# Kernel tuning notes

Hardware: AMD Instinct MI355X
Metric: run time of the kernel (lower is better)

The kernel has to match this reference:

```python
import jax, jax.numpy as jnp
import numpy as np

D_MODEL = 2048
H = 16
D_K = D_MODEL // H


def setup_inputs() -> dict:
    key = jax.random.key(0)
    ks = jax.random.split(key, 9)
    b, n, d = 2, 2048, D_MODEL
    s = 1.0 / np.sqrt(d)
    return {
        "x": jax.random.normal(ks[0], (b, n, d), jnp.float32),
        "Wq": jax.random.normal(ks[1], (d, d), jnp.float32) * s,
        "bq": jax.random.normal(ks[2], (d,), jnp.float32) * 0.01,
        "Wk": jax.random.normal(ks[3], (d, d), jnp.float32) * s,
        "bk": jax.random.normal(ks[4], (d,), jnp.float32) * 0.01,
        "Wv": jax.random.normal(ks[5], (d, d), jnp.float32) * s,
        "bv": jax.random.normal(ks[6], (d,), jnp.float32) * 0.01,
        "Wo": jax.random.normal(ks[7], (d, d), jnp.float32) * s,
        "bo": jax.random.normal(ks[8], (d,), jnp.float32) * 0.01,
    }


def reference(x, Wq, bq, Wk, bk, Wv, bv, Wo, bo):
    b, n, d = x.shape
    h, dk = H, D_K

    def split_heads(t):
        return t.reshape(b, n, h, dk).transpose(0, 2, 1, 3)  # (b,h,n,dk)

    q = split_heads(x @ Wq + bq)
    k = split_heads(x @ Wk + bk)
    v = split_heads(x @ Wv + bv)

    scores = jnp.einsum("bhqd,bhkd->bhqk", q, k) / jnp.sqrt(jnp.float32(dk))
    causal = jnp.tril(jnp.ones((n, n), dtype=bool))  # (n,n)
    scores = jnp.where(causal[None, None], scores, -jnp.inf)
    attn = jax.nn.softmax(scores, axis=-1)  # dropout = identity (eval)

    out = jnp.einsum("bhqk,bhkd->bhqd", attn, v)
    out = out.transpose(0, 2, 1, 3).reshape(b, n, d)
    return out @ Wo + bo
```

## Files before the change

kernel.cpp:

```cpp
#include <hip/hip_runtime.h>

typedef unsigned short u16;
typedef unsigned int u32;
typedef __attribute__((ext_vector_type(8))) short short8;
typedef __attribute__((ext_vector_type(4))) float f32x4;
typedef __attribute__((ext_vector_type(16))) float f32x16;
typedef __attribute__((ext_vector_type(4))) u16 u16x4;
typedef __attribute__((ext_vector_type(4))) u32 u32x4;

#define QK_SCALE 0.12751736915185197f

__device__ __forceinline__ u16 f2bf(float f) {
  u32 u = __builtin_bit_cast(u32, f);
  u = u + 0x7FFFu + ((u >> 16) & 1u);
  return (u16)(u >> 16);
}

__device__ __forceinline__ void async_copy16(const void* g, void* l) {
  __builtin_amdgcn_global_load_lds(
      (const __attribute__((address_space(1))) u32*)g,
      (__attribute__((address_space(3))) u32*)l, 16, 0, 0);
}

#define VMCNT(n) asm volatile("s_waitcnt vmcnt(" #n ")" ::: "memory")

__global__ __launch_bounds__(256) void cast_x_kernel(const float* __restrict__ x,
                                                     u16* __restrict__ xb, int n) {
  int i = (blockIdx.x * 256 + threadIdx.x) * 8;
  if (i >= n) return;
  float4 a = *(const float4*)(x + i);
  float4 b = *(const float4*)(x + i + 4);
  short8 o;
  o[0] = (short)f2bf(a.x); o[1] = (short)f2bf(a.y);
  o[2] = (short)f2bf(a.z); o[3] = (short)f2bf(a.w);
  o[4] = (short)f2bf(b.x); o[5] = (short)f2bf(b.y);
  o[6] = (short)f2bf(b.z); o[7] = (short)f2bf(b.w);
  *(short8*)(xb + i) = o;
}

__global__ __launch_bounds__(256) void transW_kernel(
    const float* __restrict__ W0, const float* __restrict__ W1,
    const float* __restrict__ W2, const float* __restrict__ W3,
    u16* __restrict__ O0, u16* __restrict__ O1, u16* __restrict__ O2, u16* __restrict__ O3) {
  const float* Ws[4] = {W0, W1, W2, W3};
  u16* Os[4] = {O0, O1, O2, O3};
  const float* W = Ws[blockIdx.z];
  u16* O = Os[blockIdx.z];

  __shared__ float T[64][65];
  int t = threadIdx.x;
  int k0 = blockIdx.y * 64, n0 = blockIdx.x * 64;
  int r = t >> 4, c = (t & 15) * 4;
#pragma unroll
  for (int i = 0; i < 4; ++i) {
    float4 v = *(const float4*)&W[(size_t)(k0 + r + i * 16) * 2048 + n0 + c];
    T[r + i * 16][c + 0] = v.x; T[r + i * 16][c + 1] = v.y;
    T[r + i * 16][c + 2] = v.z; T[r + i * 16][c + 3] = v.w;
  }
  __syncthreads();
#pragma unroll
  for (int i = 0; i < 4; ++i) {
    int nn = r + i * 16;
    u16x4 o;
    o[0] = f2bf(T[c + 0][nn]); o[1] = f2bf(T[c + 1][nn]);
    o[2] = f2bf(T[c + 2][nn]); o[3] = f2bf(T[c + 3][nn]);
    *(u16x4*)&O[(size_t)(n0 + nn) * 2048 + k0 + c] = o;
  }
}

__global__ __launch_bounds__(256) void transV_kernel(const u16* __restrict__ V,
                                                     u16* __restrict__ Vt) {
  int bh = blockIdx.y;
  int n0 = blockIdx.x * 64;
  const u16* Vb = V + (size_t)bh * 262144;
  u16* Ob = Vt + (size_t)bh * 262144;
  __shared__ u16 T[64 * 129];
  int t = threadIdx.x;
#pragma unroll
  for (int j = 0; j < 4; ++j) {
    int p = t + j * 256;
    int r = p >> 4, c = (p & 15) * 8;
    short8 v = *(const short8*)(Vb + (size_t)(n0 + r) * 128 + c);
#pragma unroll
    for (int e = 0; e < 8; ++e) T[r * 129 + c + e] = (u16)v[e];
  }
  __syncthreads();
#pragma unroll
  for (int pass = 0; pass < 4; ++pass) {
    int dk = (t >> 3) + pass * 32;
    int cn = (t & 7) * 8;
    short8 o;
#pragma unroll
    for (int e = 0; e < 8; ++e) o[e] = (short)T[(cn + e) * 129 + dk];
    *(short8*)(Ob + (size_t)dk * 2048 + n0 + cn) = o;
  }
}

__global__ __launch_bounds__(512, 2) void gemm256_kernel(
    const u16* __restrict__ A, const u16* __restrict__ W,
    const float* __restrict__ b0, const float* __restrict__ b1, const float* __restrict__ b2,
    u16* __restrict__ oq, u16* __restrict__ ok, u16* __restrict__ ov) {
  __shared__ __align__(16) u16 SM[65536];

  int t = threadIdx.x;
  int lane = t & 63, w = t >> 6;
  int wm = w >> 2, wn = w & 3;
  int g = lane >> 4, lr = lane & 15;
  int m0 = blockIdx.y * 256, n0 = blockIdx.x * 256;

  const u16* AsrcB = A + (size_t)(m0 + (t >> 3)) * 2048 + ((t & 7) ^ ((t >> 3) & 7)) * 8;
  const u16* BsrcB = W + (size_t)(n0 + (t >> 3)) * 2048 + ((t & 7) ^ ((t >> 3) & 7)) * 8;
  int t8 = t * 8;

  int ko0 = (g ^ (lr & 7)) * 8;
  int ko1 = ((4 + g) ^ (lr & 7)) * 8;
  int aoff[8], boff[4];
#pragma unroll
  for (int mf = 0; mf < 8; ++mf) aoff[mf] = (wm * 128 + mf * 16 + lr) * 64;
#pragma unroll
  for (int nf = 0; nf < 4; ++nf) boff[nf] = (wn * 64 + nf * 16 + lr) * 64;

  f32x4 acc[8][4] = {};
  short8 af[2][2], bfr[4][2];

#define SA(b, j, tl) \
  async_copy16(AsrcB + (size_t)(j) * 131072 + (tl) * 64, (void*)(SM + (b) * 32768 + (j) * 4096 + t8))
#define SB(b, j, tl) \
  async_copy16(BsrcB + (size_t)(j) * 131072 + (tl) * 64, \
               (void*)(SM + (b) * 32768 + 16384 + (j) * 4096 + t8))

#define PHASE(hbuf, q, STAGE_OPS, VM_OP)                                        \
  {                                                                             \
    const u16* Ab = SM + (hbuf) * 32768;                                        \
    const u16* Bb = Ab + 16384;                                                 \
    af[0][0] = *(const short8*)&Ab[aoff[2 * (q)] + ko0];                        \
    af[0][1] = *(const short8*)&Ab[aoff[2 * (q)] + ko1];                        \
    af[1][0] = *(const short8*)&Ab[aoff[2 * (q) + 1] + ko0];                    \
    af[1][1] = *(const short8*)&Ab[aoff[2 * (q) + 1] + ko1];                    \
    if ((q) == 0) {                                                             \
      _Pragma("unroll") for (int nf = 0; nf < 4; ++nf) {                        \
        bfr[nf][0] = *(const short8*)&Bb[boff[nf] + ko0];                       \
        bfr[nf][1] = *(const short8*)&Bb[boff[nf] + ko1];                       \
      }                                                                         \
    }                                                                           \
    STAGE_OPS;                                                                  \
    __builtin_amdgcn_s_barrier();                                               \
    asm volatile("s_waitcnt lgkmcnt(0)" ::: "memory");                          \
    __builtin_amdgcn_sched_barrier(0);                                          \
    __builtin_amdgcn_s_setprio(1);                                              \
    _Pragma("unroll") for (int kk = 0; kk < 2; ++kk)                            \
        _Pragma("unroll") for (int m2 = 0; m2 < 2; ++m2)                        \
            _Pragma("unroll") for (int nf = 0; nf < 4; ++nf)                    \
                acc[2 * (q) + m2][nf] = __builtin_amdgcn_mfma_f32_16x16x32_bf16(\
                    af[m2][kk], bfr[nf][kk], acc[2 * (q) + m2][nf], 0, 0, 0);   \
    __builtin_amdgcn_s_setprio(0);                                              \
    VM_OP;                                                                      \
    __builtin_amdgcn_s_barrier();                                               \
  }

  SB(0, 0, 0); SB(0, 1, 0); SB(0, 2, 0); SB(0, 3, 0);
  SA(0, 0, 0); SA(0, 2, 0); SA(0, 1, 0); SA(0, 3, 0);
  SB(1, 0, 1); SB(1, 1, 1); SB(1, 2, 1); SB(1, 3, 1);
  SA(1, 0, 1); SA(1, 2, 1);
  VMCNT(6);
  __builtin_amdgcn_s_barrier();

  for (int i = 0; i < 16; ++i) {
    bool more = i < 15;
    int t1 = 2 * i + 1, t2 = 2 * i + 2, t3 = 2 * i + 3;
    PHASE(0, 0, { SA(1, 1, t1); SA(1, 3, t1); }, {});
    PHASE(0, 1, { if (more) { SB(0, 0, t2); SB(0, 1, t2); } }, {});
    PHASE(0, 2, { if (more) { SB(0, 2, t2); SB(0, 3, t2); } }, {});
    PHASE(0, 3, { if (more) { SA(0, 0, t2); SA(0, 2, t2); } },
          { if (more) { VMCNT(6); } else { VMCNT(0); } });
    PHASE(1, 0, { if (more) { SA(0, 1, t2); SA(0, 3, t2); } }, {});
    PHASE(1, 1, { if (more) { SB(1, 0, t3); SB(1, 1, t3); } }, {});
    PHASE(1, 2, { if (more) { SB(1, 2, t3); SB(1, 3, t3); } }, {});
    PHASE(1, 3, { if (more) { SA(1, 0, t3); SA(1, 2, t3); } },
          { if (more) { VMCNT(6); } else { VMCNT(0); } });
  }
#undef PHASE
#undef SA
#undef SB

  int zsel = n0 >> 11;
  const float* bias = (zsel == 0) ? b0 : (zsel == 1) ? b1 : b2;
  u16* outb = (zsel == 0) ? oq : (zsel == 1) ? ok : ov;
#pragma unroll
  for (int mf = 0; mf < 8; ++mf) {
#pragma unroll
    for (int nf = 0; nf < 4; ++nf) {
      int col = n0 + wn * 64 + nf * 16 + lr;
      int cc = col & 2047;
      float bv = bias[cc];
#pragma unroll
      for (int i = 0; i < 4; ++i) {
        int rr = m0 + wm * 128 + mf * 16 + 4 * g + i;
        float v = acc[mf][nf][i] + bv;
        int b = rr >> 11, np = rr & 2047, h = cc >> 7, dk = cc & 127;
        outb[((size_t)(b * 16 + h) * 2048 + np) * 128 + dk] = f2bf(v);
      }
    }
  }
}

__global__ __launch_bounds__(512, 2) void gemmO_kernel(
    const u16* __restrict__ A, const u16* __restrict__ W,
    const float* __restrict__ bias, float* __restrict__ of) {
  __shared__ __align__(16) u16 SM[73728];

  int t = threadIdx.x;
  int lane = t & 63, w = t >> 6;
  int wm = w >> 2, wn = w & 3;
  int g = lane >> 4, lr = lane & 15;
  int m0 = blockIdx.y * 128, n0 = blockIdx.x * 256;

  int sArow = ((t >> 8) << 6) + ((t >> 3) & 31);
  int c8A = (t & 7) ^ ((t >> 3) & 7);
  const u16* Asrc = A + (size_t)(m0 + sArow) * 2048 + c8A * 8;
  int rB = t >> 3;
  int c8B = (t & 7) ^ (rB & 7);
  const u16* Bsrc = W + (size_t)(n0 + rB) * 2048 + c8B * 8;

  int ko0 = (g ^ (lr & 7)) * 8;
  int ko1 = ((4 + g) ^ (lr & 7)) * 8;
  int offA[4], offB[4];
#pragma unroll
  for (int mf = 0; mf < 4; ++mf)
    offA[mf] = (mf >> 1) * 4096 + wm * 2048 + ((mf & 1) * 16 + lr) * 64;
#pragma unroll
  for (int nf = 0; nf < 4; ++nf)
    offB[nf] = 8192 + (wn >> 1) * 8192 + ((wn & 1) * 64 + nf * 16 + lr) * 64;

  f32x4 acc[4][4] = {};

#define STG_A(sbuf, mh, kt) \
  async_copy16(Asrc + (mh) * 65536 + (kt), (void*)(SM + (sbuf) + (mh) * 4096 + t * 8))
#define STG_B(sbuf, half, kt)                                                 \
  do {                                                                        \
    async_copy16(Bsrc + (half) * 262144 + (kt),                               \
                 (void*)(SM + (sbuf) + 8192 + (half) * 8192 + t * 8));        \
    async_copy16(Bsrc + (half) * 262144 + 131072 + (kt),                      \
                 (void*)(SM + (sbuf) + 8192 + (half) * 8192 + 4096 + t * 8)); \
  } while (0)

  STG_A(0, 0, 0); STG_B(0, 0, 0);
  STG_A(0, 1, 0); STG_B(0, 1, 0);
  STG_A(24576, 0, 64); STG_B(24576, 0, 64);
  STG_A(24576, 1, 64); STG_B(24576, 1, 64);
  VMCNT(6);
  __builtin_amdgcn_s_barrier();

  u32 cb = 0, sb = 49152;
  for (int tt = 0; tt < 32; ++tt) {
    int kt2 = (tt + 2) << 6;
    bool stg = tt < 30;
    const u16* Bu = SM + cb;

    short8 af[2][2], bfr[4][2];
#pragma unroll
    for (int m2 = 0; m2 < 2; ++m2) {
      af[m2][0] = *(const short8*)&Bu[offA[m2] + ko0];
      af[m2][1] = *(const short8*)&Bu[offA[m2] + ko1];
    }
#pragma unroll
    for (int nf = 0; nf < 4; ++nf) {
      bfr[nf][0] = *(const short8*)&Bu[offB[nf] + ko0];
      bfr[nf][1] = *(const short8*)&Bu[offB[nf] + ko1];
    }
    if (stg) { STG_A(sb, 0, kt2); STG_B(sb, 0, kt2); }
    __builtin_amdgcn_s_barrier();
    asm volatile("s_waitcnt lgkmcnt(0)" ::: "memory");
    __builtin_amdgcn_sched_barrier(0);
    __builtin_amdgcn_s_setprio(1);
#pragma unroll
    for (int kk = 0; kk < 2; ++kk)
#pragma unroll
      for (int m2 = 0; m2 < 2; ++m2)
#pragma unroll
        for (int nf = 0; nf < 4; ++nf)
          acc[m2][nf] =
              __builtin_amdgcn_mfma_f32_16x16x32_bf16(af[m2][kk], bfr[nf][kk], acc[m2][nf], 0, 0, 0);
    __builtin_amdgcn_s_setprio(0);
    __builtin_amdgcn_s_barrier();

#pragma unroll
    for (int m2 = 0; m2 < 2; ++m2) {
      af[m2][0] = *(const short8*)&Bu[offA[2 + m2] + ko0];
      af[m2][1] = *(const short8*)&Bu[offA[2 + m2] + ko1];
    }
    if (stg) { STG_A(sb, 1, kt2); STG_B(sb, 1, kt2); }
    __builtin_amdgcn_s_barrier();
    asm volatile("s_waitcnt lgkmcnt(0)" ::: "memory");
    __builtin_amdgcn_sched_barrier(0);
    __builtin_amdgcn_s_setprio(1);
#pragma unroll
    for (int kk = 0; kk < 2; ++kk)
#pragma unroll
      for (int m2 = 0; m2 < 2; ++m2)
#pragma unroll
        for (int nf = 0; nf < 4; ++nf)
          acc[2 + m2][nf] = __builtin_amdgcn_mfma_f32_16x16x32_bf16(af[m2][kk], bfr[nf][kk],
                                                                    acc[2 + m2][nf], 0, 0, 0);
    __builtin_amdgcn_s_setprio(0);
    if (tt < 30) { VMCNT(6); } else { VMCNT(0); }
    __builtin_amdgcn_s_barrier();

    cb += 24576; if (cb == 73728) cb = 0;
    sb += 24576; if (sb == 73728) sb = 0;
  }
#undef STG_A
#undef STG_B

#pragma unroll
  for (int mf = 0; mf < 4; ++mf) {
#pragma unroll
    for (int nf = 0; nf < 4; ++nf) {
      int col = n0 + wn * 64 + nf * 16 + lr;
      float bv = bias[col];
#pragma unroll
      for (int i = 0; i < 4; ++i) {
        int rr = m0 + wm * 64 + mf * 16 + 4 * g + i;
        of[(size_t)rr * 2048 + col] = acc[mf][nf][i] + bv;
      }
    }
  }
}

__global__ __launch_bounds__(256, 2) void attn_kernel(
    const u16* __restrict__ Q, const u16* __restrict__ K, const u16* __restrict__ Vt,
    u16* __restrict__ ctx) {
  int bh = blockIdx.y;
  int q0 = (int)(gridDim.x - 1 - blockIdx.x) * 128;
  int t = threadIdx.x, lane = t & 63, w = t >> 6;
  int h = lane >> 5;
  int ql = lane & 31;
  int q0w = q0 + w * 32;
  int qg = q0w + ql;

  const u16* Qb = Q + (size_t)bh * 262144;
  const u16* Kb = K + (size_t)bh * 262144;
  const u16* Vb = Vt + (size_t)bh * 262144;

  __shared__ __align__(16) u16 SM[32768];

  short8 qf[8];
  {
    const u16* qrow = Qb + (size_t)qg * 128 + 8 * h;
#pragma unroll
    for (int kk = 0; kk < 8; ++kk) qf[kk] = *(const short8*)(qrow + 16 * kk);
  }

  f32x16 acc[4] = {};
  float m = -1e30f, lsum = 0.f;

  int nt = (q0 + 128) >> 6;
  int wave_max = q0w + 31;

  auto STAGE = [&](int buf, int kv0) {
    u16* Ksb = SM + buf * 16384;
    u16* Vsb = Ksb + 8192;
#pragma unroll
    for (int it = 0; it < 4; ++it) {
      int p = t + 256 * it;
      int row = p >> 4;
      int c = (p & 15) ^ (row & 15);
      async_copy16(Kb + (size_t)(kv0 + row) * 128 + c * 8, (void*)(Ksb + p * 8));
      async_copy16(Vb + (size_t)(2 * row + (c >> 3)) * 2048 + kv0 + (c & 7) * 8,
                   (void*)(Vsb + p * 8));
    }
  };

  STAGE(0, 0);
  __syncthreads();

  for (int step = 0; step < nt; ++step) {
    int kv0 = step << 6;
    int cur = step & 1;
    if (step + 1 < nt) STAGE(cur ^ 1, (step + 1) << 6);

    if (kv0 <= wave_max) {
      const u16* Ksb = SM + cur * 16384;
      const u16* Vsb = Ksb + 8192;

      f32x16 s0 = {}, s1 = {};
#pragma unroll
      for (int kk = 0; kk < 8; ++kk) {
        int c = (2 * kk + h) ^ (ql & 15);
        short8 kf0 = *(const short8*)&Ksb[ql * 128 + c * 8];
        s0 = __builtin_amdgcn_mfma_f32_32x32x16_bf16(kf0, qf[kk], s0, 0, 0, 0);
        short8 kf1 = *(const short8*)&Ksb[(32 + ql) * 128 + c * 8];
        s1 = __builtin_amdgcn_mfma_f32_32x32x16_bf16(kf1, qf[kk], s1, 0, 0, 0);
      }

      if (kv0 + 63 > q0w) {
#pragma unroll
        for (int r = 0; r < 16; ++r) {
          int slot = (r & 3) + 8 * (r >> 2) + 4 * h;
          if (kv0 + slot > qg) s0[r] = -1e30f;
          if (kv0 + 32 + slot > qg) s1[r] = -1e30f;
        }
      }

      float tm = fmaxf(s0[0], s1[0]);
#pragma unroll
      for (int r = 1; r < 16; ++r) tm = fmaxf(tm, fmaxf(s0[r], s1[r]));
      tm = fmaxf(tm, __shfl_xor(tm, 32));
      tm *= QK_SCALE;

      if (__any(tm > m + 8.0f)) {
        float mn = fmaxf(m, tm);
        float rr = exp2f(m - mn);
        m = mn;
        lsum *= rr;
#pragma unroll
        for (int d = 0; d < 4; ++d)
#pragma unroll
          for (int i = 0; i < 16; ++i) acc[d][i] *= rr;
      }

      float rs = 0.f;
#pragma unroll
      for (int r = 0; r < 16; ++r) {
        s0[r] = exp2f(fmaf(s0[r], QK_SCALE, -m));
        s1[r] = exp2f(fmaf(s1[r], QK_SCALE, -m));
        rs += s0[r] + s1[r];
      }
      rs += __shfl_xor(rs, 32);
      lsum += rs;

      u32 up0[8], up1[8];
#pragma unroll
      for (int mi = 0; mi < 8; ++mi) {
        asm("v_cvt_pk_bf16_f32 %0, %1, %2" : "=v"(up0[mi]) : "v"(s0[2 * mi]), "v"(s0[2 * mi + 1]));
        asm("v_cvt_pk_bf16_f32 %0, %1, %2" : "=v"(up1[mi]) : "v"(s1[2 * mi]), "v"(s1[2 * mi + 1]));
      }

#pragma unroll
      for (int g16 = 0; g16 < 4; ++g16) {
        int Qd = g16 & 1;
        u32 c0 = (g16 < 2) ? up0[4 * Qd + 0] : up1[4 * Qd + 0];
        u32 c1 = (g16 < 2) ? up0[4 * Qd + 1] : up1[4 * Qd + 1];
        u32 c2 = (g16 < 2) ? up0[4 * Qd + 2] : up1[4 * Qd + 2];
        u32 c3 = (g16 < 2) ? up0[4 * Qd + 3] : up1[4 * Qd + 3];
        u32 d0 = __shfl_xor(c0, 32), d1 = __shfl_xor(c1, 32);
        u32 d2 = __shfl_xor(c2, 32), d3 = __shfl_xor(c3, 32);
        u32x4 paw;
        paw[0] = h ? d2 : c0;
        paw[1] = h ? d3 : c1;
        paw[2] = h ? c2 : d0;
        paw[3] = h ? c3 : d1;
        short8 pa = __builtin_bit_cast(short8, paw);
#pragma unroll
        for (int d = 0; d < 4; ++d) {
          int dk = 32 * d + ql;
          int prow = dk >> 1;
          int lch = (dk & 1) * 8 + 2 * g16 + h;
          int slot = lch ^ (prow & 15);
          short8 vf = *(const short8*)&Vsb[prow * 128 + slot * 8];
          acc[d] = __builtin_amdgcn_mfma_f32_32x32x16_bf16(vf, pa, acc[d], 0, 0, 0);
        }
      }
    }
    __syncthreads();
  }

  u16* Ot = SM + w * 4352;
  float inv = 1.f / lsum;
#pragma unroll
  for (int d = 0; d < 4; ++d)
#pragma unroll
    for (int r = 0; r < 16; ++r) {
      int dk = 32 * d + (r & 3) + 8 * (r >> 2) + 4 * h;
      Ot[ql * 136 + dk] = f2bf(acc[d][r] * inv);
    }
  __syncthreads();
  int b = bh >> 4, hh = bh & 15;
#pragma unroll
  for (int it = 0; it < 8; ++it) {
    int p = lane + 64 * it;
    int row = p >> 4, ch = p & 15;
    short8 v = *(const short8*)&Ot[row * 136 + ch * 8];
    *(short8*)(ctx + ((size_t)(b * 2048 + q0 + w * 32 + row)) * 2048 + hh * 128 + ch * 8) = v;
  }
}

extern "C" void kernel_launch(void* const* d_in, const int* in_sizes, int n_in,
                              void* d_out, int out_size, void* d_ws, size_t ws_size,
                              hipStream_t stream) {
  const float* x = (const float*)d_in[0];
  const float* Wq = (const float*)d_in[1];
  const float* bq = (const float*)d_in[2];
  const float* Wk = (const float*)d_in[3];
  const float* bk = (const float*)d_in[4];
  const float* Wv = (const float*)d_in[5];
  const float* bv = (const float*)d_in[6];
  const float* Wo = (const float*)d_in[7];
  const float* bo = (const float*)d_in[8];
  float* out = (float*)d_out;

  u16* xb = (u16*)d_ws;
  u16* WTq = xb + 8388608;
  u16* WTk = WTq + 4194304;
  u16* WTv = WTk + 4194304;
  u16* WTo = WTv + 4194304;
  u16* Qs = WTo + 4194304;
  u16* Ks = Qs + 8388608;
  u16* Vs = Ks + 8388608;
  u16* ctx = Vs + 8388608;
  u16* Vt = xb;

  cast_x_kernel<<<4096, 256, 0, stream>>>(x, xb, 8388608);
  transW_kernel<<<dim3(32, 32, 4), 256, 0, stream>>>(Wq, Wk, Wv, Wo, WTq, WTk, WTv, WTo);
  gemm256_kernel<<<dim3(24, 16), 512, 0, stream>>>(xb, WTq, bq, bk, bv, Qs, Ks, Vs);
  transV_kernel<<<dim3(32, 32), 256, 0, stream>>>(Vs, Vt);
  attn_kernel<<<dim3(16, 32), 256, 0, stream>>>(Qs, Ks, Vt, ctx);
  gemmO_kernel<<<dim3(8, 32), 512, 0, stream>>>(ctx, WTo, bo, out);
}
```

Before: 266.3 us.

## Fuse V transpose into QKV GEMM epilogue and vectorize output stores via LDS

Removes the separate transV kernel by having the QKV GEMM epilogue stage each tile in shared memory and write V directly in transposed (dk-major) layout, while Q and K tiles now go out as 16-byte vector stores instead of scalar bf16 writes. Launch bounds drop to one block per SM to fit the larger LDS buffer. The attention kernel also raises wave priority around its MFMA loops. This saves a kernel launch and a full read/write pass over V, at the cost of lower GEMM occupancy and an extra LDS round trip in the epilogue.

```diff
diff --git a/kernel.cpp b/kernel.cpp
--- a/kernel.cpp
+++ b/kernel.cpp
@@ -68,39 +68,11 @@
   }
 }
 
-__global__ __launch_bounds__(256) void transV_kernel(const u16* __restrict__ V,
-                                                     u16* __restrict__ Vt) {
-  int bh = blockIdx.y;
-  int n0 = blockIdx.x * 64;
-  const u16* Vb = V + (size_t)bh * 262144;
-  u16* Ob = Vt + (size_t)bh * 262144;
-  __shared__ u16 T[64 * 129];
-  int t = threadIdx.x;
-#pragma unroll
-  for (int j = 0; j < 4; ++j) {
-    int p = t + j * 256;
-    int r = p >> 4, c = (p & 15) * 8;
-    short8 v = *(const short8*)(Vb + (size_t)(n0 + r) * 128 + c);
-#pragma unroll
-    for (int e = 0; e < 8; ++e) T[r * 129 + c + e] = (u16)v[e];
-  }
-  __syncthreads();
-#pragma unroll
-  for (int pass = 0; pass < 4; ++pass) {
-    int dk = (t >> 3) + pass * 32;
-    int cn = (t & 7) * 8;
-    short8 o;
-#pragma unroll
-    for (int e = 0; e < 8; ++e) o[e] = (short)T[(cn + e) * 129 + dk];
-    *(short8*)(Ob + (size_t)dk * 2048 + n0 + cn) = o;
-  }
-}
-
-__global__ __launch_bounds__(512, 2) void gemm256_kernel(
+__global__ __launch_bounds__(512, 1) void gemm256_kernel(
     const u16* __restrict__ A, const u16* __restrict__ W,
     const float* __restrict__ b0, const float* __restrict__ b1, const float* __restrict__ b2,
-    u16* __restrict__ oq, u16* __restrict__ ok, u16* __restrict__ ov) {
-  __shared__ __align__(16) u16 SM[65536];
+    u16* __restrict__ oq, u16* __restrict__ ok, u16* __restrict__ ovt) {
+  __shared__ __align__(16) u16 SM[67584];
 
   int t = threadIdx.x;
   int lane = t & 63, w = t >> 6;
@@ -185,21 +157,47 @@
 
   int zsel = n0 >> 11;
   const float* bias = (zsel == 0) ? b0 : (zsel == 1) ? b1 : b2;
-  u16* outb = (zsel == 0) ? oq : (zsel == 1) ? ok : ov;
+  bool isV = (zsel == 2);
+
 #pragma unroll
   for (int mf = 0; mf < 8; ++mf) {
 #pragma unroll
     for (int nf = 0; nf < 4; ++nf) {
-      int col = n0 + wn * 64 + nf * 16 + lr;
-      int cc = col & 2047;
-      float bv = bias[cc];
+      int colc = wn * 64 + nf * 16 + lr;
+      float bv = bias[(n0 + colc) & 2047];
 #pragma unroll
       for (int i = 0; i < 4; ++i) {
-        int rr = m0 + wm * 128 + mf * 16 + 4 * g + i;
-        float v = acc[mf][nf][i] + bv;
-        int b = rr >> 11, np = rr & 2047, h = cc >> 7, dk = cc & 127;
-        outb[((size_t)(b * 16 + h) * 2048 + np) * 128 + dk] = f2bf(v);
-      }
+        int token = wm * 128 + mf * 16 + 4 * g + i;
+        u16 v = f2bf(acc[mf][nf][i] + bv);
+        if (isV) SM[colc * 264 + token] = v;
+        else SM[token * 264 + colc] = v;
+      }
+    }
+  }
+  __syncthreads();
+
+  if (!isV) {
+    u16* outb = (zsel == 0) ? oq : ok;
+#pragma unroll
+    for (int it = 0; it < 16; ++it) {
+      int id = t + 512 * it;
+      int token = id >> 5, c8 = (id & 31) * 8;
+      short8 v = *(const short8*)&SM[token * 264 + c8];
+      int rr = m0 + token;
+      int colg = ((n0 + c8) & 2047);
+      int b = rr >> 11, np = rr & 2047, h = colg >> 7, dk = colg & 127;
+      *(short8*)&outb[((size_t)(b * 16 + h) * 2048 + np) * 128 + dk] = v;
+    }
+  } else {
+#pragma unroll
+    for (int it = 0; it < 16; ++it) {
+      int id = t + 512 * it;
+      int colc = id >> 5, t8k = (id & 31) * 8;
+      short8 v = *(const short8*)&SM[colc * 264 + t8k];
+      int rr = m0 + t8k;
+      int vcol = (n0 - 4096) + colc;
+      int b = rr >> 11, np = rr & 2047, h = vcol >> 7, dk = vcol & 127;
+      *(short8*)&ovt[(((size_t)(b * 16 + h) * 128 + dk) * 2048) + np] = v;
     }
   }
 }
@@ -384,6 +382,7 @@
       const u16* Vsb = Ksb + 8192;
 
       f32x16 s0 = {}, s1 = {};
+      __builtin_amdgcn_s_setprio(1);
 #pragma unroll
       for (int kk = 0; kk < 8; ++kk) {
         int c = (2 * kk + h) ^ (ql & 15);
@@ -392,6 +391,7 @@
         short8 kf1 = *(const short8*)&Ksb[(32 + ql) * 128 + c * 8];
         s1 = __builtin_amdgcn_mfma_f32_32x32x16_bf16(kf1, qf[kk], s1, 0, 0, 0);
       }
+      __builtin_amdgcn_s_setprio(0);
 
       if (kv0 + 63 > q0w) {
 #pragma unroll
@@ -451,6 +451,7 @@
         paw[2] = h ? c2 : d0;
         paw[3] = h ? c3 : d1;
         short8 pa = __builtin_bit_cast(short8, paw);
+        __builtin_amdgcn_s_setprio(1);
 #pragma unroll
         for (int d = 0; d < 4; ++d) {
           int dk = 32 * d + ql;
@@ -460,6 +461,7 @@
           short8 vf = *(const short8*)&Vsb[prow * 128 + slot * 8];
           acc[d] = __builtin_amdgcn_mfma_f32_32x32x16_bf16(vf, pa, acc[d], 0, 0, 0);
         }
+        __builtin_amdgcn_s_setprio(0);
       }
     }
     __syncthreads();
@@ -506,14 +508,12 @@
   u16* WTo = WTv + 4194304;
   u16* Qs = WTo + 4194304;
   u16* Ks = Qs + 8388608;
-  u16* Vs = Ks + 8388608;
-  u16* ctx = Vs + 8388608;
-  u16* Vt = xb;
+  u16* Vt = Ks + 8388608;
+  u16* ctx = Vt + 8388608;
 
   cast_x_kernel<<<4096, 256, 0, stream>>>(x, xb, 8388608);
   transW_kernel<<<dim3(32, 32, 4), 256, 0, stream>>>(Wq, Wk, Wv, Wo, WTq, WTk, WTv, WTo);
-  gemm256_kernel<<<dim3(24, 16), 512, 0, stream>>>(xb, WTq, bq, bk, bv, Qs, Ks, Vs);
-  transV_kernel<<<dim3(32, 32), 256, 0, stream>>>(Vs, Vt);
+  gemm256_kernel<<<dim3(24, 16), 512, 0, stream>>>(xb, WTq, bq, bk, bv, Qs, Ks, Vt);
   attn_kernel<<<dim3(16, 32), 256, 0, stream>>>(Qs, Ks, Vt, ctx);
   gemmO_kernel<<<dim3(8, 32), 512, 0, stream>>>(ctx, WTo, bo, out);
 }
```

Measured after the change: 266.4 us. About the same (+0.0%).
